# Kernel tuning notes

Hardware: AMD Instinct MI355X
Metric: run time of the kernel (lower is better)

## Reference

```python
import jax, jax.numpy as jnp
import numpy as np
from jax import lax

N_LAYERS = 30
KERNEL = 5
MU = 255.0  # quantization_channels=256 -> mu = 255
DILATIONS = [(2 ** k) % 10 for k in range(N_LAYERS)]  # 2^k mod (n_layers/n_cycles)


def causal_conv1d(x, w, b, dilation):
    # x: [B,1,T], w: [1,1,K], b: [1]; left-pad so output is causal, same length.
    pad = (w.shape[-1] - 1) * dilation
    xp = jnp.pad(x, ((0, 0), (0, 0), (pad, 0)))
    y = lax.conv_general_dilated(xp, w, window_strides=(1,), padding='VALID',
                                 rhs_dilation=(dilation,),
                                 dimension_numbers=('NCH', 'OIH', 'NCH'))
    return y + b[None, :, None]


def setup_inputs() -> dict:
    key = jax.random.key(0)
    ks = jax.random.split(key, 12)
    B, T = 8, 262144
    s = 0.2  # keep gated activations away from saturation
    return {
        'x': jax.random.normal(ks[0], (B, 1, T), dtype=jnp.float32),
        'causal_w': jax.random.normal(ks[1], (1, 1, KERNEL), jnp.float32) * s,
        'causal_b': jnp.zeros((1,), jnp.float32),
        'filter_w': jax.random.normal(ks[2], (N_LAYERS, 1, 1, KERNEL), jnp.float32) * s,
        'filter_b': jax.random.normal(ks[3], (N_LAYERS, 1), jnp.float32) * s,
        'gate_w': jax.random.normal(ks[4], (N_LAYERS, 1, 1, KERNEL), jnp.float32) * s,
        'gate_b': jax.random.normal(ks[5], (N_LAYERS, 1), jnp.float32) * s,
        'res_w': jax.random.normal(ks[6], (N_LAYERS, 1, 1, 1), jnp.float32) * s,
        'res_b': jax.random.normal(ks[7], (N_LAYERS, 1), jnp.float32) * s,
        'conv1_w': jax.random.normal(ks[8], (1, 1, 1), jnp.float32) * s,
        'conv1_b': jnp.zeros((1,), jnp.float32),
        'conv2_w': jax.random.normal(ks[9], (1, 1, 1), jnp.float32) * s,
        'conv2_b': jnp.zeros((1,), jnp.float32),
    }


def reference(x, causal_w, causal_b, filter_w, filter_b, gate_w, gate_b,
              res_w, res_b, conv1_w, conv1_b, conv2_w, conv2_b):
    h = causal_conv1d(x, causal_w, causal_b, 1)
    skip_sum = jnp.zeros_like(h)
    for k in range(N_LAYERS):  # fixed small layer loop; dilation is static per layer
        d = DILATIONS[k]
        f = jnp.tanh(causal_conv1d(h, filter_w[k], filter_b[k], d))
        g = jax.nn.sigmoid(causal_conv1d(h, gate_w[k], gate_b[k], d))
        z = f * g
        skip_sum = skip_sum + z
        # 1x1 residual conv (1 channel) = scale + bias, then residual add
        h = z * res_w[k][0, 0, 0] + res_b[k][0] + h
    out = jax.nn.relu(skip_sum) * conv1_w[0, 0, 0] + conv1_b[0]
    out = jax.nn.relu(out) * conv2_w[0, 0, 0] + conv2_b[0]
    # mu-law expanding
    out = jnp.sign(out) * (jnp.power(1.0 + MU, jnp.abs(out)) - 1.0) / MU
    return jax.nn.softmax(out, axis=-1)
```

## Files before the change

### kernel.cpp

```cpp
#include <hip/hip_runtime.h>
#include <cmath>

#define T_LEN 262144
#define NROW 8
#define NL 30
#define NT 512
#define PPT 4
#define EXT (NT * PPT * 2)
#define HALO 576
#define TILE (EXT - HALO)
#define PB ((T_LEN + TILE - 1) / TILE)
#define PAD 32
#define CH 4096
#define RB (T_LEN / CH)
#define NB2 (NROW * RB)

#define NEG2LOG2E -2.885390082f
#define NEGLOG2E  -1.4426950409f

#if __has_builtin(__builtin_amdgcn_exp2f)
#define EXP2(x) __builtin_amdgcn_exp2f(x)
#else
#define EXP2(x) __expf(0.6931471805599453f * (x))
#endif

__device__ __forceinline__ float fast_rcp(float x) { return __builtin_amdgcn_rcpf(x); }

__device__ const int c_cut[NL] = {
      8,  16,  32,  64,  88,  96, 112, 144, 168, 176,
    192, 224, 248, 256, 272, 304, 328, 336, 352, 384,
    408, 416, 432, 464, 488, 496, 512, 544, 568, 576};

__device__ __forceinline__ float gated(float af, float ag)
{
    const float u = EXP2(af * NEG2LOG2E);
    const float w = EXP2(ag * NEGLOG2E);
    return (1.0f - u) * fast_rcp((1.0f + u) * (1.0f + w));
}

template<int D>
__device__ __forceinline__ void layer_pair(
    int k, int cut,
    const float* __restrict__ fw, const float* __restrict__ fb,
    const float* __restrict__ gw, const float* __restrict__ gb,
    const float* __restrict__ rw, const float* __restrict__ rb,
    const float* __restrict__ src, float* __restrict__ dst,
    float2 (&h)[PPT], float2 (&skip)[PPT], int tid, bool writeback)
{
    const float f0 = fw[k*5+0], f1 = fw[k*5+1], f2 = fw[k*5+2], f3 = fw[k*5+3], f4 = fw[k*5+4];
    const float fbk = fb[k];
    const float g0 = gw[k*5+0], g1 = gw[k*5+1], g2 = gw[k*5+2], g3 = gw[k*5+3], g4 = gw[k*5+4];
    const float gbk = gb[k];
    const float rwk = rw[k], rbk = rb[k];

    #pragma unroll
    for (int p = 0; p < PPT; ++p) {
        const int i2 = 2 * (tid + p * NT);
        if (p == 0 && (i2 + 1) < cut) continue;

        const float2 v0 = *(const float2*)&src[i2 - 4*D];
        const float2 v1 = *(const float2*)&src[i2 - 3*D];
        const float2 v2 = *(const float2*)&src[i2 - 2*D];
        const float2 v3 = *(const float2*)&src[i2 -   D];
        const float2 v4 = h[p];

        float afx = fbk, afy = fbk;
        afx = fmaf(f0, v0.x, afx); afy = fmaf(f0, v0.y, afy);
        afx = fmaf(f1, v1.x, afx); afy = fmaf(f1, v1.y, afy);
        afx = fmaf(f2, v2.x, afx); afy = fmaf(f2, v2.y, afy);
        afx = fmaf(f3, v3.x, afx); afy = fmaf(f3, v3.y, afy);
        afx = fmaf(f4, v4.x, afx); afy = fmaf(f4, v4.y, afy);
        float agx = gbk, agy = gbk;
        agx = fmaf(g0, v0.x, agx); agy = fmaf(g0, v0.y, agy);
        agx = fmaf(g1, v1.x, agx); agy = fmaf(g1, v1.y, agy);
        agx = fmaf(g2, v2.x, agx); agy = fmaf(g2, v2.y, agy);
        agx = fmaf(g3, v3.x, agx); agy = fmaf(g3, v3.y, agy);
        agx = fmaf(g4, v4.x, agx); agy = fmaf(g4, v4.y, agy);

        const float zx = gated(afx, agx);
        const float zy = gated(afy, agy);
        skip[p].x += zx; skip[p].y += zy;
        h[p].x = fmaf(zx, rwk, rbk) + v4.x;
        h[p].y = fmaf(zy, rwk, rbk) + v4.y;
        if (writeback) *(float2*)&dst[i2] = h[p];
    }
    if (writeback) __syncthreads();
}

__device__ __forceinline__ void layer_pair_d1(
    int k,
    const float* __restrict__ fw, const float* __restrict__ fb,
    const float* __restrict__ gw, const float* __restrict__ gb,
    const float* __restrict__ rw, const float* __restrict__ rb,
    const float* __restrict__ src, float* __restrict__ dst,
    float2 (&h)[PPT], float2 (&skip)[PPT], int tid)
{
    const float f0 = fw[k*5+0], f1 = fw[k*5+1], f2 = fw[k*5+2], f3 = fw[k*5+3], f4 = fw[k*5+4];
    const float fbk = fb[k];
    const float g0 = gw[k*5+0], g1 = gw[k*5+1], g2 = gw[k*5+2], g3 = gw[k*5+3], g4 = gw[k*5+4];
    const float gbk = gb[k];
    const float rwk = rw[k], rbk = rb[k];

    #pragma unroll
    for (int p = 0; p < PPT; ++p) {
        const int i2 = 2 * (tid + p * NT);
        const float2 a = *(const float2*)&src[i2 - 4];
        const float2 b = *(const float2*)&src[i2 - 2];
        const float2 c = h[p];

        float afx = fbk, afy = fbk, agx = gbk, agy = gbk;
        afx = fmaf(f0, a.x, afx); afy = fmaf(f0, a.y, afy);
        afx = fmaf(f1, a.y, afx); afy = fmaf(f1, b.x, afy);
        afx = fmaf(f2, b.x, afx); afy = fmaf(f2, b.y, afy);
        afx = fmaf(f3, b.y, afx); afy = fmaf(f3, c.x, afy);
        afx = fmaf(f4, c.x, afx); afy = fmaf(f4, c.y, afy);
        agx = fmaf(g0, a.x, agx); agy = fmaf(g0, a.y, agy);
        agx = fmaf(g1, a.y, agx); agy = fmaf(g1, b.x, agy);
        agx = fmaf(g2, b.x, agx); agy = fmaf(g2, b.y, agy);
        agx = fmaf(g3, b.y, agx); agy = fmaf(g3, c.x, agy);
        agx = fmaf(g4, c.x, agx); agy = fmaf(g4, c.y, agy);

        const float zx = gated(afx, agx);
        const float zy = gated(afy, agy);
        skip[p].x += zx; skip[p].y += zy;
        h[p].x = fmaf(zx, rwk, rbk) + c.x;
        h[p].y = fmaf(zy, rwk, rbk) + c.y;
        *(float2*)&dst[i2] = h[p];
    }
    __syncthreads();
}

__global__ __launch_bounds__(NT, 8)
void k_wavenet(const float* __restrict__ x,
               const float* __restrict__ cw,  const float* __restrict__ cb,
               const float* __restrict__ fw,  const float* __restrict__ fb,
               const float* __restrict__ gw,  const float* __restrict__ gb,
               const float* __restrict__ rw,  const float* __restrict__ rb,
               const float* __restrict__ c1w, const float* __restrict__ c1b,
               const float* __restrict__ c2w, const float* __restrict__ c2b,
               float* __restrict__ eout, float* __restrict__ partsum)
{
    __shared__ float hrawA[PAD + EXT];
    __shared__ float hrawB[PAD + EXT];
    __shared__ float reds[NT / 64];
    float* bufA = hrawA + PAD;
    float* bufB = hrawB + PAD;

    const int tid  = threadIdx.x;
    const int row  = blockIdx.x / PB;
    const int tile = blockIdx.x % PB;
    const int t0   = tile * TILE;

    if (tid < PAD) { hrawA[tid] = 0.0f; hrawB[tid] = 0.0f; }

    const float* xr = x + (size_t)row * T_LEN;
    float2 h[PPT], skip[PPT];
    #pragma unroll
    for (int p = 0; p < PPT; ++p) {
        const int i2 = 2 * (tid + p * NT);
        const int g = t0 - HALO + i2;
        float2 v;
        v.x = (g     >= 0 && g     < T_LEN) ? xr[g]     : 0.0f;
        v.y = (g + 1 >= 0 && g + 1 < T_LEN) ? xr[g + 1] : 0.0f;
        *(float2*)&bufA[i2] = v;
        h[p] = v;
        skip[p].x = 0.0f; skip[p].y = 0.0f;
    }
    __syncthreads();

    {
        const float w0 = cw[0], w1 = cw[1], w2 = cw[2], w3 = cw[3], w4 = cw[4];
        const float b  = cb[0];
        #pragma unroll
        for (int p = 0; p < PPT; ++p) {
            const int i2 = 2 * (tid + p * NT);
            const float2 a = *(const float2*)&bufA[i2 - 4];
            const float2 bb = *(const float2*)&bufA[i2 - 2];
            const float2 c = h[p];
            float ax = b, ay = b;
            ax = fmaf(w0, a.x, ax);  ay = fmaf(w0, a.y, ay);
            ax = fmaf(w1, a.y, ax);  ay = fmaf(w1, bb.x, ay);
            ax = fmaf(w2, bb.x, ax); ay = fmaf(w2, bb.y, ay);
            ax = fmaf(w3, bb.y, ax); ay = fmaf(w3, c.x, ay);
            ax = fmaf(w4, c.x, ax);  ay = fmaf(w4, c.y, ay);
            h[p].x = ax; h[p].y = ay;
        }
        #pragma unroll
        for (int p = 0; p < PPT; ++p)
            *(float2*)&bufB[2 * (tid + p * NT)] = h[p];
        __syncthreads();
    }

    layer_pair_d1(0, fw, fb, gw, gb, rw, rb, bufB, bufA, h, skip, tid);
    int k = 1;
    #pragma unroll 1
    for (int c = 0; c < 7; ++c) {
        layer_pair<2>(k+0, c_cut[k+0], fw, fb, gw, gb, rw, rb, bufA, bufB, h, skip, tid, true);
        layer_pair<4>(k+1, c_cut[k+1], fw, fb, gw, gb, rw, rb, bufB, bufA, h, skip, tid, true);
        layer_pair<8>(k+2, c_cut[k+2], fw, fb, gw, gb, rw, rb, bufA, bufB, h, skip, tid, true);
        layer_pair<6>(k+3, c_cut[k+3], fw, fb, gw, gb, rw, rb, bufB, bufA, h, skip, tid, true);
        k += 4;
    }
    layer_pair<2>(29, c_cut[29], fw, fb, gw, gb, rw, rb, bufA, bufB, h, skip, tid, false);

    const float w1 = c1w[0], b1 = c1b[0], w2 = c2w[0], b2 = c2b[0];
    float s = 0.0f;
    float* er = eout + (size_t)row * T_LEN;
    #pragma unroll
    for (int p = 0; p < PPT; ++p) {
        const int i2 = 2 * (tid + p * NT);
        if (i2 >= HALO) {
            const int t = t0 + i2 - HALO;
            if (t < T_LEN) {
                float ox = fmaf(fmaxf(skip[p].x, 0.0f), w1, b1);
                float oy = fmaf(fmaxf(skip[p].y, 0.0f), w1, b1);
                ox = fmaf(fmaxf(ox, 0.0f), w2, b2);
                oy = fmaf(fmaxf(oy, 0.0f), w2, b2);
                float vx = fmaf(EXP2(8.0f * fabsf(ox)), (1.0f/255.0f), -(1.0f/255.0f));
                float vy = fmaf(EXP2(8.0f * fabsf(oy)), (1.0f/255.0f), -(1.0f/255.0f));
                vx = copysignf(vx, ox);
                vy = copysignf(vy, oy);
                const float ex = __expf(vx);
                const float ey = __expf(vy);
                float2 e; e.x = ex; e.y = ey;
                *(float2*)&er[t] = e;
                s += ex + ey;
            }
        }
    }
    #pragma unroll
    for (int off = 32; off >= 1; off >>= 1) s += __shfl_xor(s, off, 64);
    if ((tid & 63) == 0) reds[tid >> 6] = s;
    __syncthreads();
    if (tid == 0) {
        float ss = 0.0f;
        #pragma unroll
        for (int w = 0; w < NT / 64; ++w) ss += reds[w];
        partsum[blockIdx.x] = ss;
    }
}

__global__ __launch_bounds__(256)
void k_scale(float* __restrict__ ebuf, const float* __restrict__ partsum)
{
    const int tid = threadIdx.x;
    const int row = blockIdx.x / RB;

    __shared__ float red[4];
    float s = 0.0f;
    for (int j = tid; j < PB; j += 256) s += partsum[row * PB + j];
    #pragma unroll
    for (int off = 32; off >= 1; off >>= 1) s += __shfl_xor(s, off, 64);
    if ((tid & 63) == 0) red[tid >> 6] = s;
    __syncthreads();
    const float tot = (red[0] + red[1]) + (red[2] + red[3]);
    const float inv = 1.0f / tot;

    float4* vp = (float4*)(ebuf + (size_t)blockIdx.x * CH);
    #pragma unroll
    for (int q = 0; q < 4; ++q) {
        float4 v = vp[tid + q * 256];
        v.x *= inv; v.y *= inv; v.z *= inv; v.w *= inv;
        vp[tid + q * 256] = v;
    }
}

extern "C" void kernel_launch(void* const* d_in, const int* in_sizes, int n_in,
                              void* d_out, int out_size, void* d_ws, size_t ws_size,
                              hipStream_t stream)
{
    const float* x   = (const float*)d_in[0];
    const float* cw  = (const float*)d_in[1];
    const float* cb  = (const float*)d_in[2];
    const float* fw  = (const float*)d_in[3];
    const float* fb  = (const float*)d_in[4];
    const float* gw  = (const float*)d_in[5];
    const float* gb  = (const float*)d_in[6];
    const float* rw  = (const float*)d_in[7];
    const float* rb  = (const float*)d_in[8];
    const float* c1w = (const float*)d_in[9];
    const float* c1b = (const float*)d_in[10];
    const float* c2w = (const float*)d_in[11];
    const float* c2b = (const float*)d_in[12];

    float* eout    = (float*)d_out;
    float* partsum = (float*)d_ws;

    k_wavenet<<<NROW * PB, NT, 0, stream>>>(x, cw, cb, fw, fb, gw, gb, rw, rb,
                                            c1w, c1b, c2w, c2b, eout, partsum);
    k_scale<<<NB2, 256, 0, stream>>>(eout, partsum);
}
```

Before: 155.1 us.

## Vectorize layer math with packed float2 ops, fully unroll layers, retune block shape

Rewrites the per-layer convolution and gating math using ext_vector_type float2 so the compiler can emit packed FP32 instructions (v_pk_fma/v_pk_mul). It fully unrolls the 30 layers with compile-time dilation, cut and writeback flags, which drops the constant-memory cut table and the runtime loop. The last layer skips computing h since it is not needed. Block shape changes from 512 threads x 4 pairs to 256 threads x 6 pairs, which alters tile size, halo overhead and occupancy, and full unrolling raises code size and register pressure.

```diff
diff --git a/kernel.cpp b/kernel.cpp
--- a/kernel.cpp
+++ b/kernel.cpp
@@ -4,8 +4,8 @@
 #define T_LEN 262144
 #define NROW 8
 #define NL 30
-#define NT 512
-#define PPT 4
+#define NT 256
+#define PPT 6
 #define EXT (NT * PPT * 2)
 #define HALO 576
 #define TILE (EXT - HALO)
@@ -24,28 +24,25 @@
 #define EXP2(x) __expf(0.6931471805599453f * (x))
 #endif
 
+typedef float f32x2 __attribute__((ext_vector_type(2)));
+
 __device__ __forceinline__ float fast_rcp(float x) { return __builtin_amdgcn_rcpf(x); }
 
-__device__ const int c_cut[NL] = {
-      8,  16,  32,  64,  88,  96, 112, 144, 168, 176,
-    192, 224, 248, 256, 272, 304, 328, 336, 352, 384,
-    408, 416, 432, 464, 488, 496, 512, 544, 568, 576};
-
-__device__ __forceinline__ float gated(float af, float ag)
-{
-    const float u = EXP2(af * NEG2LOG2E);
-    const float w = EXP2(ag * NEGLOG2E);
-    return (1.0f - u) * fast_rcp((1.0f + u) * (1.0f + w));
-}
-
-template<int D>
-__device__ __forceinline__ void layer_pair(
-    int k, int cut,
+__device__ __forceinline__ f32x2 exp2v(f32x2 x) {
+    f32x2 r; r.x = EXP2(x.x); r.y = EXP2(x.y); return r;
+}
+__device__ __forceinline__ f32x2 rcpv(f32x2 x) {
+    f32x2 r; r.x = fast_rcp(x.x); r.y = fast_rcp(x.y); return r;
+}
+
+template<int D, int CUT, bool WB>
+__device__ __forceinline__ void layerv(
+    int k,
     const float* __restrict__ fw, const float* __restrict__ fb,
     const float* __restrict__ gw, const float* __restrict__ gb,
     const float* __restrict__ rw, const float* __restrict__ rb,
     const float* __restrict__ src, float* __restrict__ dst,
-    float2 (&h)[PPT], float2 (&skip)[PPT], int tid, bool writeback)
+    f32x2 (&h)[PPT], f32x2 (&skip)[PPT], int tid)
 {
     const float f0 = fw[k*5+0], f1 = fw[k*5+1], f2 = fw[k*5+2], f3 = fw[k*5+3], f4 = fw[k*5+4];
     const float fbk = fb[k];
@@ -56,81 +53,90 @@
     #pragma unroll
     for (int p = 0; p < PPT; ++p) {
         const int i2 = 2 * (tid + p * NT);
-        if (p == 0 && (i2 + 1) < cut) continue;
-
-        const float2 v0 = *(const float2*)&src[i2 - 4*D];
-        const float2 v1 = *(const float2*)&src[i2 - 3*D];
-        const float2 v2 = *(const float2*)&src[i2 - 2*D];
-        const float2 v3 = *(const float2*)&src[i2 -   D];
-        const float2 v4 = h[p];
-
-        float afx = fbk, afy = fbk;
-        afx = fmaf(f0, v0.x, afx); afy = fmaf(f0, v0.y, afy);
-        afx = fmaf(f1, v1.x, afx); afy = fmaf(f1, v1.y, afy);
-        afx = fmaf(f2, v2.x, afx); afy = fmaf(f2, v2.y, afy);
-        afx = fmaf(f3, v3.x, afx); afy = fmaf(f3, v3.y, afy);
-        afx = fmaf(f4, v4.x, afx); afy = fmaf(f4, v4.y, afy);
-        float agx = gbk, agy = gbk;
-        agx = fmaf(g0, v0.x, agx); agy = fmaf(g0, v0.y, agy);
-        agx = fmaf(g1, v1.x, agx); agy = fmaf(g1, v1.y, agy);
-        agx = fmaf(g2, v2.x, agx); agy = fmaf(g2, v2.y, agy);
-        agx = fmaf(g3, v3.x, agx); agy = fmaf(g3, v3.y, agy);
-        agx = fmaf(g4, v4.x, agx); agy = fmaf(g4, v4.y, agy);
-
-        const float zx = gated(afx, agx);
-        const float zy = gated(afy, agy);
-        skip[p].x += zx; skip[p].y += zy;
-        h[p].x = fmaf(zx, rwk, rbk) + v4.x;
-        h[p].y = fmaf(zy, rwk, rbk) + v4.y;
-        if (writeback) *(float2*)&dst[i2] = h[p];
-    }
-    if (writeback) __syncthreads();
-}
-
-__device__ __forceinline__ void layer_pair_d1(
-    int k,
+        if (2 * p * NT < CUT) {
+            if ((i2 + 1) < CUT) continue;
+        }
+
+        const f32x2 v0 = *(const f32x2*)&src[i2 - 4*D];
+        const f32x2 v1 = *(const f32x2*)&src[i2 - 3*D];
+        const f32x2 v2 = *(const f32x2*)&src[i2 - 2*D];
+        const f32x2 v3 = *(const f32x2*)&src[i2 -   D];
+        const f32x2 v4 = h[p];
+
+        f32x2 af = fbk + f0 * v0;
+        af = f1 * v1 + af;
+        af = f2 * v2 + af;
+        af = f3 * v3 + af;
+        af = f4 * v4 + af;
+        f32x2 ag = gbk + g0 * v0;
+        ag = g1 * v1 + ag;
+        ag = g2 * v2 + ag;
+        ag = g3 * v3 + ag;
+        ag = g4 * v4 + ag;
+
+        const f32x2 u = exp2v(af * NEG2LOG2E);
+        const f32x2 w = exp2v(ag * NEGLOG2E);
+        const f32x2 num = 1.0f - u;
+        const f32x2 den = (1.0f + u) * (1.0f + w);
+        const f32x2 z = num * rcpv(den);
+        skip[p] += z;
+        if (WB) {
+            h[p] = (z * rwk + rbk) + v4;
+            *(f32x2*)&dst[i2] = h[p];
+        }
+    }
+    if (WB) __syncthreads();
+}
+
+__device__ __forceinline__ void layer_d1(
     const float* __restrict__ fw, const float* __restrict__ fb,
     const float* __restrict__ gw, const float* __restrict__ gb,
     const float* __restrict__ rw, const float* __restrict__ rb,
     const float* __restrict__ src, float* __restrict__ dst,
-    float2 (&h)[PPT], float2 (&skip)[PPT], int tid)
-{
-    const float f0 = fw[k*5+0], f1 = fw[k*5+1], f2 = fw[k*5+2], f3 = fw[k*5+3], f4 = fw[k*5+4];
-    const float fbk = fb[k];
-    const float g0 = gw[k*5+0], g1 = gw[k*5+1], g2 = gw[k*5+2], g3 = gw[k*5+3], g4 = gw[k*5+4];
-    const float gbk = gb[k];
-    const float rwk = rw[k], rbk = rb[k];
+    f32x2 (&h)[PPT], f32x2 (&skip)[PPT], int tid)
+{
+    const float f0 = fw[0], f1 = fw[1], f2 = fw[2], f3 = fw[3], f4 = fw[4];
+    const float fbk = fb[0];
+    const float g0 = gw[0], g1 = gw[1], g2 = gw[2], g3 = gw[3], g4 = gw[4];
+    const float gbk = gb[0];
+    const float rwk = rw[0], rbk = rb[0];
 
     #pragma unroll
     for (int p = 0; p < PPT; ++p) {
         const int i2 = 2 * (tid + p * NT);
-        const float2 a = *(const float2*)&src[i2 - 4];
-        const float2 b = *(const float2*)&src[i2 - 2];
-        const float2 c = h[p];
-
-        float afx = fbk, afy = fbk, agx = gbk, agy = gbk;
-        afx = fmaf(f0, a.x, afx); afy = fmaf(f0, a.y, afy);
-        afx = fmaf(f1, a.y, afx); afy = fmaf(f1, b.x, afy);
-        afx = fmaf(f2, b.x, afx); afy = fmaf(f2, b.y, afy);
-        afx = fmaf(f3, b.y, afx); afy = fmaf(f3, c.x, afy);
-        afx = fmaf(f4, c.x, afx); afy = fmaf(f4, c.y, afy);
-        agx = fmaf(g0, a.x, agx); agy = fmaf(g0, a.y, agy);
-        agx = fmaf(g1, a.y, agx); agy = fmaf(g1, b.x, agy);
-        agx = fmaf(g2, b.x, agx); agy = fmaf(g2, b.y, agy);
-        agx = fmaf(g3, b.y, agx); agy = fmaf(g3, c.x, agy);
-        agx = fmaf(g4, c.x, agx); agy = fmaf(g4, c.y, agy);
-
-        const float zx = gated(afx, agx);
-        const float zy = gated(afy, agy);
-        skip[p].x += zx; skip[p].y += zy;
-        h[p].x = fmaf(zx, rwk, rbk) + c.x;
-        h[p].y = fmaf(zy, rwk, rbk) + c.y;
-        *(float2*)&dst[i2] = h[p];
+        const f32x2 a = *(const f32x2*)&src[i2 - 4];
+        const f32x2 b = *(const f32x2*)&src[i2 - 2];
+        const f32x2 c = h[p];
+        f32x2 v0, v1, v2, v3;
+        v0.x = a.x; v0.y = a.y;
+        v1.x = a.y; v1.y = b.x;
+        v2.x = b.x; v2.y = b.y;
+        v3.x = b.y; v3.y = c.x;
+
+        f32x2 af = fbk + f0 * v0;
+        af = f1 * v1 + af;
+        af = f2 * v2 + af;
+        af = f3 * v3 + af;
+        af = f4 * c  + af;
+        f32x2 ag = gbk + g0 * v0;
+        ag = g1 * v1 + ag;
+        ag = g2 * v2 + ag;
+        ag = g3 * v3 + ag;
+        ag = g4 * c  + ag;
+
+        const f32x2 u = exp2v(af * NEG2LOG2E);
+        const f32x2 w = exp2v(ag * NEGLOG2E);
+        const f32x2 num = 1.0f - u;
+        const f32x2 den = (1.0f + u) * (1.0f + w);
+        const f32x2 z = num * rcpv(den);
+        skip[p] += z;
+        h[p] = (z * rwk + rbk) + c;
+        *(f32x2*)&dst[i2] = h[p];
     }
     __syncthreads();
 }
 
-__global__ __launch_bounds__(NT, 8)
+__global__ __launch_bounds__(NT, 6)
 void k_wavenet(const float* __restrict__ x,
                const float* __restrict__ cw,  const float* __restrict__ cb,
                const float* __restrict__ fw,  const float* __restrict__ fb,
@@ -140,8 +146,8 @@
                const float* __restrict__ c2w, const float* __restrict__ c2b,
                float* __restrict__ eout, float* __restrict__ partsum)
 {
-    __shared__ float hrawA[PAD + EXT];
-    __shared__ float hrawB[PAD + EXT];
+    __shared__ __align__(16) float hrawA[PAD + EXT];
+    __shared__ __align__(16) float hrawB[PAD + EXT];
     __shared__ float reds[NT / 64];
     float* bufA = hrawA + PAD;
     float* bufB = hrawB + PAD;
@@ -154,15 +160,15 @@
     if (tid < PAD) { hrawA[tid] = 0.0f; hrawB[tid] = 0.0f; }
 
     const float* xr = x + (size_t)row * T_LEN;
-    float2 h[PPT], skip[PPT];
+    f32x2 h[PPT], skip[PPT];
     #pragma unroll
     for (int p = 0; p < PPT; ++p) {
         const int i2 = 2 * (tid + p * NT);
         const int g = t0 - HALO + i2;
-        float2 v;
+        f32x2 v;
         v.x = (g     >= 0 && g     < T_LEN) ? xr[g]     : 0.0f;
         v.y = (g + 1 >= 0 && g + 1 < T_LEN) ? xr[g + 1] : 0.0f;
-        *(float2*)&bufA[i2] = v;
+        *(f32x2*)&bufA[i2] = v;
         h[p] = v;
         skip[p].x = 0.0f; skip[p].y = 0.0f;
     }
@@ -174,34 +180,55 @@
         #pragma unroll
         for (int p = 0; p < PPT; ++p) {
             const int i2 = 2 * (tid + p * NT);
-            const float2 a = *(const float2*)&bufA[i2 - 4];
-            const float2 bb = *(const float2*)&bufA[i2 - 2];
-            const float2 c = h[p];
-            float ax = b, ay = b;
-            ax = fmaf(w0, a.x, ax);  ay = fmaf(w0, a.y, ay);
-            ax = fmaf(w1, a.y, ax);  ay = fmaf(w1, bb.x, ay);
-            ax = fmaf(w2, bb.x, ax); ay = fmaf(w2, bb.y, ay);
-            ax = fmaf(w3, bb.y, ax); ay = fmaf(w3, c.x, ay);
-            ax = fmaf(w4, c.x, ax);  ay = fmaf(w4, c.y, ay);
-            h[p].x = ax; h[p].y = ay;
+            const f32x2 a  = *(const f32x2*)&bufA[i2 - 4];
+            const f32x2 bb = *(const f32x2*)&bufA[i2 - 2];
+            const f32x2 c  = h[p];
+            f32x2 v0, v1, v2, v3;
+            v0.x = a.x;  v0.y = a.y;
+            v1.x = a.y;  v1.y = bb.x;
+            v2.x = bb.x; v2.y = bb.y;
+            v3.x = bb.y; v3.y = c.x;
+            f32x2 acc = b + w0 * v0;
+            acc = w1 * v1 + acc;
+            acc = w2 * v2 + acc;
+            acc = w3 * v3 + acc;
+            acc = w4 * c  + acc;
+            h[p] = acc;
+            *(f32x2*)&bufB[i2] = acc;
         }
-        #pragma unroll
-        for (int p = 0; p < PPT; ++p)
-            *(float2*)&bufB[2 * (tid + p * NT)] = h[p];
         __syncthreads();
     }
 
-    layer_pair_d1(0, fw, fb, gw, gb, rw, rb, bufB, bufA, h, skip, tid);
-    int k = 1;
-    #pragma unroll 1
-    for (int c = 0; c < 7; ++c) {
-        layer_pair<2>(k+0, c_cut[k+0], fw, fb, gw, gb, rw, rb, bufA, bufB, h, skip, tid, true);
-        layer_pair<4>(k+1, c_cut[k+1], fw, fb, gw, gb, rw, rb, bufB, bufA, h, skip, tid, true);
-        layer_pair<8>(k+2, c_cut[k+2], fw, fb, gw, gb, rw, rb, bufA, bufB, h, skip, tid, true);
-        layer_pair<6>(k+3, c_cut[k+3], fw, fb, gw, gb, rw, rb, bufB, bufA, h, skip, tid, true);
-        k += 4;
-    }
-    layer_pair<2>(29, c_cut[29], fw, fb, gw, gb, rw, rb, bufA, bufB, h, skip, tid, false);
+    layer_d1(fw, fb, gw, gb, rw, rb, bufB, bufA, h, skip, tid);
+    layerv<2,  16, true >( 1, fw, fb, gw, gb, rw, rb, bufA, bufB, h, skip, tid);
+    layerv<4,  32, true >( 2, fw, fb, gw, gb, rw, rb, bufB, bufA, h, skip, tid);
+    layerv<8,  64, true >( 3, fw, fb, gw, gb, rw, rb, bufA, bufB, h, skip, tid);
+    layerv<6,  88, true >( 4, fw, fb, gw, gb, rw, rb, bufB, bufA, h, skip, tid);
+    layerv<2,  96, true >( 5, fw, fb, gw, gb, rw, rb, bufA, bufB, h, skip, tid);
+    layerv<4, 112, true >( 6, fw, fb, gw, gb, rw, rb, bufB, bufA, h, skip, tid);
+    layerv<8, 144, true >( 7, fw, fb, gw, gb, rw, rb, bufA, bufB, h, skip, tid);
+    layerv<6, 168, true >( 8, fw, fb, gw, gb, rw, rb, bufB, bufA, h, skip, tid);
+    layerv<2, 176, true >( 9, fw, fb, gw, gb, rw, rb, bufA, bufB, h, skip, tid);
+    layerv<4, 192, true >(10, fw, fb, gw, gb, rw, rb, bufB, bufA, h, skip, tid);
+    layerv<8, 224, true >(11, fw, fb, gw, gb, rw, rb, bufA, bufB, h, skip, tid);
+    layerv<6, 248, true >(12, fw, fb, gw, gb, rw, rb, bufB, bufA, h, skip, tid);
+    layerv<2, 256, true >(13, fw, fb, gw, gb, rw, rb, bufA, bufB, h, skip, tid);
+    layerv<4, 272, true >(14, fw, fb, gw, gb, rw, rb, bufB, bufA, h, skip, tid);
+    layerv<8, 304, true >(15, fw, fb, gw, gb, rw, rb, bufA, bufB, h, skip, tid);
+    layerv<6, 328, true >(16, fw, fb, gw, gb, rw, rb, bufB, bufA, h, skip, tid);
+    layerv<2, 336, true >(17, fw, fb, gw, gb, rw, rb, bufA, bufB, h, skip, tid);
+    layerv<4, 352, true >(18, fw, fb, gw, gb, rw, rb, bufB, bufA, h, skip, tid);
+    layerv<8, 384, true >(19, fw, fb, gw, gb, rw, rb, bufA, bufB, h, skip, tid);
+    layerv<6, 408, true >(20, fw, fb, gw, gb, rw, rb, bufB, bufA, h, skip, tid);
+    layerv<2, 416, true >(21, fw, fb, gw, gb, rw, rb, bufA, bufB, h, skip, tid);
+    layerv<4, 432, true >(22, fw, fb, gw, gb, rw, rb, bufB, bufA, h, skip, tid);
+    layerv<8, 464, true >(23, fw, fb, gw, gb, rw, rb, bufA, bufB, h, skip, tid);
+    layerv<6, 488, true >(24, fw, fb, gw, gb, rw, rb, bufB, bufA, h, skip, tid);
+    layerv<2, 496, true >(25, fw, fb, gw, gb, rw, rb, bufA, bufB, h, skip, tid);
+    layerv<4, 512, true >(26, fw, fb, gw, gb, rw, rb, bufB, bufA, h, skip, tid);
+    layerv<8, 544, true >(27, fw, fb, gw, gb, rw, rb, bufA, bufB, h, skip, tid);
+    layerv<6, 568, true >(28, fw, fb, gw, gb, rw, rb, bufB, bufA, h, skip, tid);
+    layerv<2, 576, false>(29, fw, fb, gw, gb, rw, rb, bufA, bufB, h, skip, tid);
 
     const float w1 = c1w[0], b1 = c1b[0], w2 = c2w[0], b2 = c2b[0];
     float s = 0.0f;
@@ -212,8 +239,9 @@
         if (i2 >= HALO) {
             const int t = t0 + i2 - HALO;
             if (t < T_LEN) {
-                float ox = fmaf(fmaxf(skip[p].x, 0.0f), w1, b1);
-                float oy = fmaf(fmaxf(skip[p].y, 0.0f), w1, b1);
+                f32x2 sk = skip[p];
+                float ox = fmaf(fmaxf(sk.x, 0.0f), w1, b1);
+                float oy = fmaf(fmaxf(sk.y, 0.0f), w1, b1);
                 ox = fmaf(fmaxf(ox, 0.0f), w2, b2);
                 oy = fmaf(fmaxf(oy, 0.0f), w2, b2);
                 float vx = fmaf(EXP2(8.0f * fabsf(ox)), (1.0f/255.0f), -(1.0f/255.0f));
@@ -222,8 +250,8 @@
                 vy = copysignf(vy, oy);
                 const float ex = __expf(vx);
                 const float ey = __expf(vy);
-                float2 e; e.x = ex; e.y = ey;
-                *(float2*)&er[t] = e;
+                f32x2 e; e.x = ex; e.y = ey;
+                *(f32x2*)&er[t] = e;
                 s += ex + ey;
             }
         }
```

Result: faster. 145.4 us (-6.3%).
